# Performance work log

Measured on AMD Instinct MI355X. Metric: run time of the kernel, lower is better.

The kernel has to match this reference:

```python
import jax, jax.numpy as jnp
import numpy as np

N = 50000      # nodes
E = 640000     # edges
D = 64         # embedding_dim
H1, H2 = 64, 128
EA = 8         # edge_attr_dim
OUT = 4
G = 64         # graphs in batch
NEG_SLOPE = 0.2  # PyG GeneralConv leaky_relu slope


def seg_softmax(a, seg, n):
    # softmax of per-edge scores a grouped by destination node seg
    m = jax.ops.segment_max(a, seg, num_segments=n)
    m = jnp.where(jnp.isfinite(m), m, 0.0)
    e = jnp.exp(a - m[seg])
    s = jax.ops.segment_sum(e, seg, num_segments=n)
    return e / (s[seg] + 1e-16)


def general_conv(h, src, dst, edge_attr, Wm, bm, We, be, att, Ws, bs, n):
    # message: lin_msg(x_j) + lin_edge(edge_attr)   [E, out]
    m = h[src] @ Wm + bm + edge_attr @ We + be
    # additive attention (heads=1): alpha = leaky_relu(<m, att>), softmax per dst
    a = jax.nn.leaky_relu(m @ att, NEG_SLOPE)
    a = seg_softmax(a, dst, n)
    msg = m * a[:, None]
    # scatter-mean aggregate
    s = jax.ops.segment_sum(msg, dst, num_segments=n)
    cnt = jax.ops.segment_sum(jnp.ones_like(a), dst, num_segments=n)
    agg = s / jnp.maximum(cnt, 1.0)[:, None]
    # skip linear on self features
    return agg + h @ Ws + bs


def setup_inputs() -> dict:
    key = jax.random.key(0)
    ks = jax.random.split(key, 24)
    rn = lambda k, shp, sc=0.05: (jax.random.normal(k, shp, jnp.float32) * sc)
    inp = {
        "x": jnp.arange(N),
        "edge_index": jax.random.randint(ks[0], (2, E), 0, N),
        "edge_attr": jax.random.normal(ks[1], (E, EA), jnp.float32),
        "batchh": jnp.sort(jax.random.randint(ks[2], (N,), 0, G)),
        "emb": rn(ks[3], (N, D), 0.1),
        # layer 0: D -> H1
        "Wm0": rn(ks[4], (D, H1)), "bm0": rn(ks[5], (H1,)),
        "We0": rn(ks[6], (EA, H1)), "be0": rn(ks[7], (H1,)),
        "att0": rn(ks[8], (H1,)),
        "Ws0": rn(ks[9], (D, H1)), "bs0": rn(ks[10], (H1,)),
        # layer 1: H1 -> H2
        "Wm1": rn(ks[11], (H1, H2)), "bm1": rn(ks[12], (H2,)),
        "We1": rn(ks[13], (EA, H2)), "be1": rn(ks[14], (H2,)),
        "att1": rn(ks[15], (H2,)),
        "Ws1": rn(ks[16], (H1, H2)), "bs1": rn(ks[17], (H2,)),
        # classifier
        "Wc1": rn(ks[18], (H2, H2)), "bc1": rn(ks[19], (H2,)),
        "Wc2": rn(ks[20], (H2, OUT)), "bc2": rn(ks[21], (OUT,)),
    }
    return inp


def reference(x, edge_index, edge_attr, batchh, emb,
              Wm0, bm0, We0, be0, att0, Ws0, bs0,
              Wm1, bm1, We1, be1, att1, Ws1, bs1,
              Wc1, bc1, Wc2, bc2):
    src, dst = edge_index[0], edge_index[1]
    h = emb[x]                                   # [N, D]
    h = jax.nn.relu(general_conv(h, src, dst, edge_attr, Wm0, bm0, We0, be0, att0, Ws0, bs0, N))
    h = jax.nn.relu(general_conv(h, src, dst, edge_attr, Wm1, bm1, We1, be1, att1, Ws1, bs1, N))
    # global mean pool per graph (dropout is identity in eval)
    s = jax.ops.segment_sum(h, batchh, num_segments=G)
    c = jax.ops.segment_sum(jnp.ones((h.shape[0],), h.dtype), batchh, num_segments=G)
    g = s / jnp.maximum(c, 1.0)[:, None]         # [G, H2]
    return jax.nn.relu(g @ Wc1 + bc1) @ Wc2 + bc2  # [G, OUT]
```

## Files before the change

kernel.cpp:

```cpp
#include <hip/hip_runtime.h>
#include <hip/hip_bf16.h>

#define DEV_INLINE __device__ __forceinline__

static constexpr int WAVE = 64;
static constexpr int EB   = 2048;
static constexpr int CAP  = 4096;
static constexpr float FP8_SCALE = 64.0f;
static constexpr float FP8_INV   = 1.0f / 64.0f;
static constexpr float EA_SCALE  = 8.0f;
static constexpr float EA_INV    = 1.0f / 8.0f;

typedef float floatx2 __attribute__((ext_vector_type(2)));
typedef unsigned int uintx4 __attribute__((ext_vector_type(4)));

DEV_INLINE float leaky02(float x) { return x > 0.f ? x : 0.2f * x; }
DEV_INLINE unsigned short f2b(float f) {
    __hip_bfloat16 b = __float2bfloat16(f);
    return *reinterpret_cast<unsigned short*>(&b);
}
DEV_INLINE float b2f(unsigned short u) {
    unsigned int x = ((unsigned int)u) << 16;
    return __uint_as_float(x);
}

__global__ __launch_bounds__(256)
void stage_kernel(const int* __restrict__ ei, const float* __restrict__ ea, int E, int nbuck,
                  const float* __restrict__ We0, const float* __restrict__ att0,
                  const float* __restrict__ be0,
                  const float* __restrict__ We1, const float* __restrict__ att1,
                  const float* __restrict__ be1,
                  int* __restrict__ bucket_cursor, unsigned int* __restrict__ staging) {
    __shared__ float swatt[32];
    __shared__ int hist[256];
    __shared__ int basesh[256];
    int tid = threadIdx.x;

    if (tid < 9) {
        float s = 0.f;
        if (tid < 8) { for (int h = 0; h < 64; ++h) s += We0[tid * 64 + h] * att0[h]; }
        else         { for (int h = 0; h < 64; ++h) s += be0[h] * att0[h]; }
        swatt[tid] = s;
    } else if (tid >= 16 && tid < 25) {
        int k = tid - 16;
        float s = 0.f;
        if (k < 8) { for (int h = 0; h < 128; ++h) s += We1[k * 128 + h] * att1[h]; }
        else       { for (int h = 0; h < 128; ++h) s += be1[h] * att1[h]; }
        swatt[tid] = s;
    }
    hist[tid] = 0;
    __syncthreads();

    int e0 = blockIdx.x * EB;
    constexpr int EPT = EB / 256;
    int rank[EPT];
    #pragma unroll
    for (int j = 0; j < EPT; ++j) {
        int e = e0 + j * 256 + tid;
        rank[j] = 0;
        if (e < E) {
            int b = ei[E + e] >> 8;
            rank[j] = atomicAdd(&hist[b], 1);
        }
    }
    __syncthreads();
    basesh[tid] = (hist[tid] > 0 && tid < nbuck) ? atomicAdd(&bucket_cursor[tid], hist[tid]) : 0;
    __syncthreads();

    #pragma unroll
    for (int j = 0; j < EPT; ++j) {
        int e = e0 + j * 256 + tid;
        if (e >= E) continue;
        int d = ei[E + e];
        int src = ei[e];
        int b = d >> 8;
        const float4* p = reinterpret_cast<const float4*>(ea + (size_t)e * 8);
        float4 a0 = p[0], a1 = p[1];
        float s0 = swatt[8]
                 + a0.x * swatt[0] + a0.y * swatt[1] + a0.z * swatt[2] + a0.w * swatt[3]
                 + a1.x * swatt[4] + a1.y * swatt[5] + a1.z * swatt[6] + a1.w * swatt[7];
        float s1 = swatt[24]
                 + a0.x * swatt[16] + a0.y * swatt[17] + a0.z * swatt[18] + a0.w * swatt[19]
                 + a1.x * swatt[20] + a1.y * swatt[21] + a1.z * swatt[22] + a1.w * swatt[23];
        int lo = 0, hi = 0;
        lo = __builtin_amdgcn_cvt_pk_fp8_f32(a0.x * EA_SCALE, a0.y * EA_SCALE, lo, false);
        lo = __builtin_amdgcn_cvt_pk_fp8_f32(a0.z * EA_SCALE, a0.w * EA_SCALE, lo, true);
        hi = __builtin_amdgcn_cvt_pk_fp8_f32(a1.x * EA_SCALE, a1.y * EA_SCALE, hi, false);
        hi = __builtin_amdgcn_cvt_pk_fp8_f32(a1.z * EA_SCALE, a1.w * EA_SCALE, hi, true);
        int pos = basesh[b] + rank[j];
        if (pos >= CAP) continue;
        uintx4 pk;
        pk[0] = (unsigned int)(src & 0xffff) | ((unsigned int)(d & 255) << 16);
        pk[1] = (unsigned int)f2b(s0) | ((unsigned int)f2b(s1) << 16);
        pk[2] = (unsigned int)lo;
        pk[3] = (unsigned int)hi;
        *reinterpret_cast<uintx4*>(staging + ((size_t)b * CAP + pos) * 4) = pk;
    }
}

__global__ __launch_bounds__(256)
void bucket_scan_kernel(const int* __restrict__ bucket_cursor, int nbuck,
                        int* __restrict__ bucket_base, int* __restrict__ csroff,
                        int N, int E) {
    __shared__ int ws2[4];
    int t = threadIdx.x, lane = t & 63, wid = t >> 6;
    int v = (t < nbuck) ? bucket_cursor[t] : 0;
    int incl = v;
    #pragma unroll
    for (int o = 1; o < 64; o <<= 1) { int u = __shfl_up(incl, o); if (lane >= o) incl += u; }
    if (lane == 63) ws2[wid] = incl;
    __syncthreads();
    int woff = 0;
    for (int w0 = 0; w0 < wid; ++w0) woff += ws2[w0];
    if (t < nbuck) bucket_base[t] = woff + incl - v;
    if (t == 0) csroff[N] = E;
}

__global__ __launch_bounds__(256)
void place_kernel(const unsigned int* __restrict__ staging,
                  const int* __restrict__ bucket_cursor, const int* __restrict__ bucket_base,
                  int* __restrict__ csroff, unsigned int* __restrict__ packed, int N) {
    __shared__ int deg[256];
    __shared__ int wsum[4];
    int b = blockIdx.x;
    int tid = threadIdx.x, lane = tid & 63, wid = tid >> 6;
    deg[tid] = 0;
    __syncthreads();
    int cnt = min(bucket_cursor[b], CAP);
    int base = bucket_base[b];
    const unsigned int* st = staging + (size_t)b * CAP * 4;

    for (int i = tid; i < cnt; i += 256) {
        unsigned int w0 = st[(size_t)i * 4];
        atomicAdd(&deg[(w0 >> 16) & 255], 1);
    }
    __syncthreads();
    int v = deg[tid];
    int incl = v;
    #pragma unroll
    for (int o = 1; o < 64; o <<= 1) { int u = __shfl_up(incl, o); if (lane >= o) incl += u; }
    if (lane == 63) wsum[wid] = incl;
    __syncthreads();
    int woff = 0;
    for (int w0 = 0; w0 < wid; ++w0) woff += wsum[w0];
    int excl = woff + incl - v;
    int node = b * 256 + tid;
    if (node < N) csroff[node] = base + excl;
    __syncthreads();
    deg[tid] = excl;
    __syncthreads();
    for (int i = tid; i < cnt; i += 256) {
        const uintx4 pk = *reinterpret_cast<const uintx4*>(st + (size_t)i * 4);
        int dl = (pk[0] >> 16) & 255;
        int pos = base + atomicAdd(&deg[dl], 1);
        *reinterpret_cast<uintx4*>(packed + (size_t)pos * 4) = pk;
    }
}

template <int H, int NB, bool INBF16>
__global__ __launch_bounds__(256)
void nodelin_kernel(const float* __restrict__ hf, const unsigned short* __restrict__ hb,
                    const int* __restrict__ xidx,
                    const float* __restrict__ Wm, const float* __restrict__ bm,
                    const float* __restrict__ Ws, const float* __restrict__ bs,
                    const float* __restrict__ att,
                    unsigned char* __restrict__ hWm8, unsigned short* __restrict__ hWsb,
                    float* __restrict__ nscore, int n) {
    constexpr int F4  = H / 4;
    constexpr int NC  = 256 / F4;
    constexpr int NPT = NB / NC;
    constexpr int LDW = 68;
    __shared__ float sh[NB][LDW];
    int n0 = blockIdx.x * NB;
    int tid = threadIdx.x;

    for (int i = tid; i < NB * 16; i += 256) {
        int node = i >> 4, q = i & 15;
        int row = n0 + node;
        float4 v = make_float4(0.f, 0.f, 0.f, 0.f);
        if (row < n) {
            if constexpr (INBF16) {
                ushort4 u = reinterpret_cast<const ushort4*>(hb + (size_t)row * 64)[q];
                v = make_float4(b2f(u.x), b2f(u.y), b2f(u.z), b2f(u.w));
            } else {
                int src = xidx ? xidx[row] : row;
                v = reinterpret_cast<const float4*>(hf + (size_t)src * 64)[q];
            }
        }
        reinterpret_cast<float4*>(&sh[node][0])[q] = v;
    }
    __syncthreads();

    int f4 = (tid % F4) * 4;
    int j0 = tid / F4;
    float4 am[NPT], as[NPT];
    float4 bm4 = *reinterpret_cast<const float4*>(bm + f4);
    float4 bs4 = *reinterpret_cast<const float4*>(bs + f4);
    #pragma unroll
    for (int p = 0; p < NPT; ++p) { am[p] = bm4; as[p] = bs4; }

    for (int k4 = 0; k4 < 16; ++k4) {
        float4 hv[NPT];
        #pragma unroll
        for (int p = 0; p < NPT; ++p)
            hv[p] = reinterpret_cast<const float4*>(&sh[j0 + p * NC][0])[k4];
        #pragma unroll
        for (int kk = 0; kk < 4; ++kk) {
            int k = k4 * 4 + kk;
            float4 wm = *reinterpret_cast<const float4*>(Wm + k * H + f4);
            float4 ws = *reinterpret_cast<const float4*>(Ws + k * H + f4);
            #pragma unroll
            for (int p = 0; p < NPT; ++p) {
                float hk = (&hv[p].x)[kk];
                am[p].x += hk * wm.x; am[p].y += hk * wm.y;
                am[p].z += hk * wm.z; am[p].w += hk * wm.w;
                as[p].x += hk * ws.x; as[p].y += hk * ws.y;
                as[p].z += hk * ws.z; as[p].w += hk * ws.w;
            }
        }
    }

    float4 at4 = *reinterpret_cast<const float4*>(att + f4);
    #pragma unroll
    for (int p = 0; p < NPT; ++p) {
        int row = n0 + j0 + p * NC;
        float sc = am[p].x * at4.x + am[p].y * at4.y + am[p].z * at4.z + am[p].w * at4.w;
        #pragma unroll
        for (int o = 1; o < F4; o <<= 1) sc += __shfl_xor(sc, o);
        if (row < n) {
            int pk = 0;
            pk = __builtin_amdgcn_cvt_pk_fp8_f32(am[p].x * FP8_SCALE, am[p].y * FP8_SCALE, pk, false);
            pk = __builtin_amdgcn_cvt_pk_fp8_f32(am[p].z * FP8_SCALE, am[p].w * FP8_SCALE, pk, true);
            *reinterpret_cast<unsigned int*>(hWm8 + (size_t)row * H + f4) = (unsigned int)pk;
            ushort4 sb;
            sb.x = f2b(as[p].x); sb.y = f2b(as[p].y); sb.z = f2b(as[p].z); sb.w = f2b(as[p].w);
            *reinterpret_cast<ushort4*>(hWsb + (size_t)row * H + f4) = sb;
            if ((tid % F4) == 0) nscore[row] = sc;
        }
    }
}

template <int H, int L>
__global__ __launch_bounds__(256)
void agg_kernel(const int* __restrict__ csr_off, const uint4* __restrict__ packed,
                const float* __restrict__ nscore,
                const float* __restrict__ We, const float* __restrict__ be,
                const unsigned char* __restrict__ hWm8, const unsigned short* __restrict__ hWsb,
                unsigned short* __restrict__ hout, int n) {
    constexpr int LSUB = (H == 128) ? 32 : 16;
    constexpr int NPW  = 64 / LSUB;
    constexpr int NPB  = NPW * 4;
    constexpr int MAXC = 64 / LSUB;
    int tid  = threadIdx.x;
    int lane = tid & 63;
    int wv   = tid >> 6;
    int sg   = lane / LSUB;
    int l    = lane % LSUB;
    int node = blockIdx.x * NPB + wv * NPW + sg;
    if (node >= n) return;
    int base = lane - l;
    int off0 = csr_off[node];
    int deg  = csr_off[node + 1] - off0;

    if (deg == 0) {
        ushort4 hs = *reinterpret_cast<const ushort4*>(hWsb + (size_t)node * H + 4 * l);
        ushort4 ob;
        ob.x = f2b(fmaxf(b2f(hs.x), 0.f));
        ob.y = f2b(fmaxf(b2f(hs.y), 0.f));
        ob.z = f2b(fmaxf(b2f(hs.z), 0.f));
        ob.w = f2b(fmaxf(b2f(hs.w), 0.f));
        *reinterpret_cast<ushort4*>(hout + (size_t)node * H + 4 * l) = ob;
        return;
    }

    float acc4[4] = {0.f, 0.f, 0.f, 0.f};
    float cea8[8] = {0.f, 0.f, 0.f, 0.f, 0.f, 0.f, 0.f, 0.f};

    auto gather_batch = [&](int se_c, float cf_c, int cnt) {
        for (int j0 = 0; j0 < cnt; j0 += 8) {
            float cj[8];
            unsigned int gj[8];
            #pragma unroll
            for (int u = 0; u < 8; ++u) {
                int j = j0 + u;
                int jj = (j < cnt) ? j : 0;
                int sj = __shfl(se_c, base + jj);
                float cf_ = __shfl(cf_c, base + jj);
                cj[u] = (j < cnt) ? cf_ : 0.f;
                gj[u] = *reinterpret_cast<const unsigned int*>(
                    hWm8 + (size_t)sj * H + 4 * l);
            }
            #pragma unroll
            for (int u = 0; u < 8; ++u) {
                floatx2 lo = __builtin_amdgcn_cvt_pk_f32_fp8(gj[u], false);
                floatx2 hi = __builtin_amdgcn_cvt_pk_f32_fp8(gj[u], true);
                acc4[0] += cj[u] * lo[0];
                acc4[1] += cj[u] * lo[1];
                acc4[2] += cj[u] * hi[0];
                acc4[3] += cj[u] * hi[1];
            }
        }
    };

    if (deg <= MAXC * LSUB) {
        int se[MAXC];
        float cf[MAXC];
        unsigned int g0[MAXC], g1[MAXC];
        float mx = -1e30f;
        #pragma unroll
        for (int c = 0; c < MAXC; ++c) {
            int i = c * LSUB + l;
            se[c] = 0; g0[c] = 0; g1[c] = 0;
            float sc = -1e30f;
            if (i < deg) {
                uint4 pk = packed[off0 + i];
                se[c] = (int)(pk.x & 0xffffu);
                float eaw = b2f((unsigned short)((pk.y >> (L * 16)) & 0xffff));
                sc = leaky02(nscore[se[c]] + eaw);
                g0[c] = pk.z; g1[c] = pk.w;
            }
            cf[c] = sc;
            mx = fmaxf(mx, sc);
        }
        #pragma unroll
        for (int o = LSUB / 2; o > 0; o >>= 1) mx = fmaxf(mx, __shfl_xor(mx, o));
        float ssum = 0.f;
        #pragma unroll
        for (int c = 0; c < MAXC; ++c) {
            int i = c * LSUB + l;
            float e = (i < deg) ? __expf(cf[c] - mx) : 0.f;
            cf[c] = e;
            ssum += e;
        }
        #pragma unroll
        for (int o = LSUB / 2; o > 0; o >>= 1) ssum += __shfl_xor(ssum, o);
        float invs = 1.f / (ssum + 1e-16f);

        #pragma unroll
        for (int c = 0; c < MAXC; ++c) {
            cf[c] *= invs;
            float cj = cf[c];
            if (cj > 0.f) {
                floatx2 p0 = __builtin_amdgcn_cvt_pk_f32_fp8(g0[c], false);
                floatx2 p1 = __builtin_amdgcn_cvt_pk_f32_fp8(g0[c], true);
                floatx2 p2 = __builtin_amdgcn_cvt_pk_f32_fp8(g1[c], false);
                floatx2 p3 = __builtin_amdgcn_cvt_pk_f32_fp8(g1[c], true);
                cea8[0] += cj * p0[0]; cea8[1] += cj * p0[1];
                cea8[2] += cj * p1[0]; cea8[3] += cj * p1[1];
                cea8[4] += cj * p2[0]; cea8[5] += cj * p2[1];
                cea8[6] += cj * p3[0]; cea8[7] += cj * p3[1];
            }
        }
        #pragma unroll
        for (int c = 0; c < MAXC; ++c) {
            int cnt = min(LSUB, deg - c * LSUB);
            gather_batch(se[c], cf[c], cnt);
            if ((c + 1) * LSUB >= deg) break;
        }
    } else {
        float mx = -1e30f;
        for (int i = l; i < deg; i += LSUB) {
            uint4 pk = packed[off0 + i];
            float eaw = b2f((unsigned short)((pk.y >> (L * 16)) & 0xffff));
            mx = fmaxf(mx, leaky02(nscore[(int)(pk.x & 0xffffu)] + eaw));
        }
        #pragma unroll
        for (int o = LSUB / 2; o > 0; o >>= 1) mx = fmaxf(mx, __shfl_xor(mx, o));
        float ssum = 0.f;
        for (int i = l; i < deg; i += LSUB) {
            uint4 pk = packed[off0 + i];
            float eaw = b2f((unsigned short)((pk.y >> (L * 16)) & 0xffff));
            ssum += __expf(leaky02(nscore[(int)(pk.x & 0xffffu)] + eaw) - mx);
        }
        #pragma unroll
        for (int o = LSUB / 2; o > 0; o >>= 1) ssum += __shfl_xor(ssum, o);
        float invs = 1.f / (ssum + 1e-16f);

        for (int c0 = 0; c0 < deg; c0 += LSUB) {
            int cnt = min(LSUB, deg - c0);
            int se = 0;
            float cf = 0.f;
            if (l < cnt) {
                uint4 pk = packed[off0 + c0 + l];
                se = (int)(pk.x & 0xffffu);
                float eaw = b2f((unsigned short)((pk.y >> (L * 16)) & 0xffff));
                cf = __expf(leaky02(nscore[se] + eaw) - mx) * invs;
                floatx2 p0 = __builtin_amdgcn_cvt_pk_f32_fp8(pk.z, false);
                floatx2 p1 = __builtin_amdgcn_cvt_pk_f32_fp8(pk.z, true);
                floatx2 p2 = __builtin_amdgcn_cvt_pk_f32_fp8(pk.w, false);
                floatx2 p3 = __builtin_amdgcn_cvt_pk_f32_fp8(pk.w, true);
                cea8[0] += cf * p0[0]; cea8[1] += cf * p0[1];
                cea8[2] += cf * p1[0]; cea8[3] += cf * p1[1];
                cea8[4] += cf * p2[0]; cea8[5] += cf * p2[1];
                cea8[6] += cf * p3[0]; cea8[7] += cf * p3[1];
            }
            gather_batch(se, cf, cnt);
        }
    }

    #pragma unroll
    for (int k = 0; k < 8; ++k) {
        float v = cea8[k];
        #pragma unroll
        for (int o = LSUB / 2; o > 0; o >>= 1) v += __shfl_xor(v, o);
        cea8[k] = v * EA_INV;
    }

    float invdeg = 1.f / (float)deg;
    ushort4 hs = *reinterpret_cast<const ushort4*>(hWsb + (size_t)node * H + 4 * l);
    float sk[4] = {b2f(hs.x), b2f(hs.y), b2f(hs.z), b2f(hs.w)};
    ushort4 ob;
    unsigned short* obp = &ob.x;
    #pragma unroll
    for (int k = 0; k < 4; ++k) {
        int f = 4 * l + k;
        float ew = be[f];
        #pragma unroll
        for (int k8 = 0; k8 < 8; ++k8) ew += cea8[k8] * We[k8 * H + f];
        float v = (acc4[k] * FP8_INV + ew) * invdeg + sk[k];
        obp[k] = f2b(fmaxf(v, 0.f));
    }
    *reinterpret_cast<ushort4*>(hout + (size_t)node * H + 4 * l) = ob;
}

__global__ __launch_bounds__(128)
void pool_sum_kernel(const unsigned short* __restrict__ h, const int* __restrict__ batchh,
                     float* __restrict__ gsum, int n) {
    int f = threadIdx.x;
    int chunk = (n + gridDim.x - 1) / gridDim.x;
    int start = blockIdx.x * chunk;
    int end = min(n, start + chunk);
    if (start >= end) return;
    float acc = 0.f;
    int cur = batchh[start];
    for (int node = start; node < end; ++node) {
        int b = batchh[node];
        if (b != cur) {
            atomicAdd(&gsum[cur * 128 + f], acc);
            acc = 0.f;
            cur = b;
        }
        acc += b2f(h[(size_t)node * 128 + f]);
    }
    atomicAdd(&gsum[cur * 128 + f], acc);
}

__global__ __launch_bounds__(128)
void classifier_kernel(const float* __restrict__ gsum, const int* __restrict__ batchh, int n,
                       const float* __restrict__ Wc1, const float* __restrict__ bc1,
                       const float* __restrict__ Wc2, const float* __restrict__ bc2,
                       float* __restrict__ out) {
    int b = blockIdx.x;
    int f = threadIdx.x;
    __shared__ float gm[128];
    __shared__ float t1[128];
    __shared__ int cnt;
    if (f == 0) {
        auto lb = [&](int key) {
            int lo = 0, hi = n;
            while (lo < hi) {
                int mid = (lo + hi) >> 1;
                if (batchh[mid] < key) lo = mid + 1; else hi = mid;
            }
            return lo;
        };
        cnt = lb(b + 1) - lb(b);
    }
    __syncthreads();
    float c = (float)max(cnt, 1);
    gm[f] = gsum[b * 128 + f] / c;
    __syncthreads();
    float acc = bc1[f];
    for (int k = 0; k < 128; ++k) acc += gm[k] * Wc1[k * 128 + f];
    t1[f] = fmaxf(acc, 0.f);
    __syncthreads();
    if (f < 4) {
        float o = bc2[f];
        for (int k = 0; k < 128; ++k) o += t1[k] * Wc2[k * 4 + f];
        out[b * 4 + f] = o;
    }
}

extern "C" void kernel_launch(void* const* d_in, const int* in_sizes, int n_in,
                              void* d_out, int out_size, void* d_ws, size_t ws_size,
                              hipStream_t stream) {
    const int* x      = (const int*)d_in[0];
    const int* ei     = (const int*)d_in[1];
    const float* ea   = (const float*)d_in[2];
    const int* batchh = (const int*)d_in[3];
    const float* emb  = (const float*)d_in[4];
    const float* Wm0 = (const float*)d_in[5];  const float* bm0 = (const float*)d_in[6];
    const float* We0 = (const float*)d_in[7];  const float* be0 = (const float*)d_in[8];
    const float* att0 = (const float*)d_in[9];
    const float* Ws0 = (const float*)d_in[10]; const float* bs0 = (const float*)d_in[11];
    const float* Wm1 = (const float*)d_in[12]; const float* bm1 = (const float*)d_in[13];
    const float* We1 = (const float*)d_in[14]; const float* be1 = (const float*)d_in[15];
    const float* att1 = (const float*)d_in[16];
    const float* Ws1 = (const float*)d_in[17]; const float* bs1 = (const float*)d_in[18];
    const float* Wc1 = (const float*)d_in[19]; const float* bc1 = (const float*)d_in[20];
    const float* Wc2 = (const float*)d_in[21]; const float* bc2 = (const float*)d_in[22];

    const int N = in_sizes[0];
    const int E = in_sizes[1] / 2;
    const int G = 64;
    const int H2 = 128;
    const int NBUCK = (N + 255) >> 8;

    char* w = (char*)d_ws;
    auto alloc = [&](size_t bytes) -> void* {
        void* p = (void*)w;
        w += (bytes + 255) & ~(size_t)255;
        return p;
    };
    unsigned short* hbuf  = (unsigned short*)alloc((size_t)N * 128 * 2);
    unsigned char* hWm8   = (unsigned char*)alloc((size_t)N * 128);
    unsigned short* hWsb  = (unsigned short*)alloc((size_t)N * 128 * 2);
    float* nscore         = (float*)alloc((size_t)N * 4);
    unsigned int* packed  = (unsigned int*)alloc((size_t)E * 16);
    unsigned int* staging = (unsigned int*)alloc((size_t)NBUCK * CAP * 16);
    int* bucket_cursor    = (int*)alloc(256 * 4);
    int* bucket_base      = (int*)alloc(256 * 4);
    int* csroff           = (int*)alloc((size_t)(N + 1) * 4);
    float* gsum           = (float*)alloc((size_t)G * H2 * 4);

    auto cdiv = [](int a, int b) { return (a + b - 1) / b; };

    (void)hipMemsetAsync(bucket_cursor, 0, 256 * 4, stream);
    (void)hipMemsetAsync(gsum, 0, (size_t)G * H2 * 4, stream);

    stage_kernel<<<cdiv(E, EB), 256, 0, stream>>>(ei, ea, E, NBUCK,
                                                  We0, att0, be0, We1, att1, be1,
                                                  bucket_cursor, staging);
    bucket_scan_kernel<<<1, 256, 0, stream>>>(bucket_cursor, NBUCK, bucket_base, csroff, N, E);
    place_kernel<<<NBUCK, 256, 0, stream>>>(staging, bucket_cursor, bucket_base,
                                            csroff, packed, N);

    nodelin_kernel<64, 64, false><<<cdiv(N, 64), 256, 0, stream>>>(
        emb, nullptr, x, Wm0, bm0, Ws0, bs0, att0, hWm8, hWsb, nscore, N);
    agg_kernel<64, 0><<<cdiv(N, 16), 256, 0, stream>>>(csroff, (const uint4*)packed, nscore,
                                                       We0, be0, hWm8, hWsb, hbuf, N);

    nodelin_kernel<128, 32, true><<<cdiv(N, 32), 256, 0, stream>>>(
        nullptr, hbuf, nullptr, Wm1, bm1, Ws1, bs1, att1, hWm8, hWsb, nscore, N);
    agg_kernel<128, 1><<<cdiv(N, 8), 256, 0, stream>>>(csroff, (const uint4*)packed, nscore,
                                                       We1, be1, hWm8, hWsb, hbuf, N);

    pool_sum_kernel<<<512, 128, 0, stream>>>(hbuf, batchh, gsum, N);
    classifier_kernel<<<G, 128, 0, stream>>>(gsum, batchh, N, Wc1, bc1, Wc2, bc2, (float*)d_out);
}
```

Before: 310.8 us.

## Fuse staging with layer-0 node linear, fold scan into place, fuse pooling into agg

Merges the edge staging kernel and the layer-0 node linear into one launch by splitting the grid between them. Each place block now computes its own bucket base with a reduction, which removes the separate scan kernel. The layer-1 aggregation now accumulates the global mean pool directly into 8 replicated per-graph sums through shared memory and atomics, so the final node features are never written and the pool kernel is gone. Launch count and global traffic drop, at the cost of extra atomics and shared-memory work in the aggregation kernel.

New measurement: 268.6 us. -13.6%, faster.

```diff
diff --git a/kernel.cpp b/kernel.cpp
--- a/kernel.cpp
+++ b/kernel.cpp
@@ -6,6 +6,7 @@
 static constexpr int WAVE = 64;
 static constexpr int EB   = 2048;
 static constexpr int CAP  = 4096;
+static constexpr int GREP = 8;
 static constexpr float FP8_SCALE = 64.0f;
 static constexpr float FP8_INV   = 1.0f / 64.0f;
 static constexpr float EA_SCALE  = 8.0f;
@@ -24,16 +25,17 @@
     return __uint_as_float(x);
 }
 
-__global__ __launch_bounds__(256)
-void stage_kernel(const int* __restrict__ ei, const float* __restrict__ ea, int E, int nbuck,
-                  const float* __restrict__ We0, const float* __restrict__ att0,
-                  const float* __restrict__ be0,
-                  const float* __restrict__ We1, const float* __restrict__ att1,
-                  const float* __restrict__ be1,
-                  int* __restrict__ bucket_cursor, unsigned int* __restrict__ staging) {
-    __shared__ float swatt[32];
-    __shared__ int hist[256];
-    __shared__ int basesh[256];
+DEV_INLINE void stage_body(char* smemraw, int bx,
+                           const int* __restrict__ ei, const float* __restrict__ ea,
+                           int E, int nbuck,
+                           const float* __restrict__ We0, const float* __restrict__ att0,
+                           const float* __restrict__ be0,
+                           const float* __restrict__ We1, const float* __restrict__ att1,
+                           const float* __restrict__ be1,
+                           int* __restrict__ bucket_cursor, unsigned int* __restrict__ staging) {
+    float* swatt = reinterpret_cast<float*>(smemraw);
+    int* hist    = reinterpret_cast<int*>(smemraw + 128);
+    int* basesh  = reinterpret_cast<int*>(smemraw + 128 + 1024);
     int tid = threadIdx.x;
 
     if (tid < 9) {
@@ -51,7 +53,7 @@
     hist[tid] = 0;
     __syncthreads();
 
-    int e0 = blockIdx.x * EB;
+    int e0 = bx * EB;
     constexpr int EPT = EB / 256;
     int rank[EPT];
     #pragma unroll
@@ -98,80 +100,21 @@
     }
 }
 
-__global__ __launch_bounds__(256)
-void bucket_scan_kernel(const int* __restrict__ bucket_cursor, int nbuck,
-                        int* __restrict__ bucket_base, int* __restrict__ csroff,
-                        int N, int E) {
-    __shared__ int ws2[4];
-    int t = threadIdx.x, lane = t & 63, wid = t >> 6;
-    int v = (t < nbuck) ? bucket_cursor[t] : 0;
-    int incl = v;
-    #pragma unroll
-    for (int o = 1; o < 64; o <<= 1) { int u = __shfl_up(incl, o); if (lane >= o) incl += u; }
-    if (lane == 63) ws2[wid] = incl;
-    __syncthreads();
-    int woff = 0;
-    for (int w0 = 0; w0 < wid; ++w0) woff += ws2[w0];
-    if (t < nbuck) bucket_base[t] = woff + incl - v;
-    if (t == 0) csroff[N] = E;
-}
-
-__global__ __launch_bounds__(256)
-void place_kernel(const unsigned int* __restrict__ staging,
-                  const int* __restrict__ bucket_cursor, const int* __restrict__ bucket_base,
-                  int* __restrict__ csroff, unsigned int* __restrict__ packed, int N) {
-    __shared__ int deg[256];
-    __shared__ int wsum[4];
-    int b = blockIdx.x;
-    int tid = threadIdx.x, lane = tid & 63, wid = tid >> 6;
-    deg[tid] = 0;
-    __syncthreads();
-    int cnt = min(bucket_cursor[b], CAP);
-    int base = bucket_base[b];
-    const unsigned int* st = staging + (size_t)b * CAP * 4;
-
-    for (int i = tid; i < cnt; i += 256) {
-        unsigned int w0 = st[(size_t)i * 4];
-        atomicAdd(&deg[(w0 >> 16) & 255], 1);
-    }
-    __syncthreads();
-    int v = deg[tid];
-    int incl = v;
-    #pragma unroll
-    for (int o = 1; o < 64; o <<= 1) { int u = __shfl_up(incl, o); if (lane >= o) incl += u; }
-    if (lane == 63) wsum[wid] = incl;
-    __syncthreads();
-    int woff = 0;
-    for (int w0 = 0; w0 < wid; ++w0) woff += wsum[w0];
-    int excl = woff + incl - v;
-    int node = b * 256 + tid;
-    if (node < N) csroff[node] = base + excl;
-    __syncthreads();
-    deg[tid] = excl;
-    __syncthreads();
-    for (int i = tid; i < cnt; i += 256) {
-        const uintx4 pk = *reinterpret_cast<const uintx4*>(st + (size_t)i * 4);
-        int dl = (pk[0] >> 16) & 255;
-        int pos = base + atomicAdd(&deg[dl], 1);
-        *reinterpret_cast<uintx4*>(packed + (size_t)pos * 4) = pk;
-    }
-}
-
 template <int H, int NB, bool INBF16>
-__global__ __launch_bounds__(256)
-void nodelin_kernel(const float* __restrict__ hf, const unsigned short* __restrict__ hb,
-                    const int* __restrict__ xidx,
-                    const float* __restrict__ Wm, const float* __restrict__ bm,
-                    const float* __restrict__ Ws, const float* __restrict__ bs,
-                    const float* __restrict__ att,
-                    unsigned char* __restrict__ hWm8, unsigned short* __restrict__ hWsb,
-                    float* __restrict__ nscore, int n) {
+DEV_INLINE void nodelin_body(char* smemraw, int bx,
+                             const float* __restrict__ hf, const unsigned short* __restrict__ hb,
+                             const int* __restrict__ xidx,
+                             const float* __restrict__ Wm, const float* __restrict__ bm,
+                             const float* __restrict__ Ws, const float* __restrict__ bs,
+                             const float* __restrict__ att,
+                             unsigned char* __restrict__ hWm8, unsigned short* __restrict__ hWsb,
+                             float* __restrict__ nscore, int n) {
     constexpr int F4  = H / 4;
     constexpr int NC  = 256 / F4;
     constexpr int NPT = NB / NC;
     constexpr int LDW = 68;
-    __shared__ float sh[NB][LDW];
-    int n0 = blockIdx.x * NB;
+    float (*sh)[LDW] = reinterpret_cast<float (*)[LDW]>(smemraw);
+    int n0 = bx * NB;
     int tid = threadIdx.x;
 
     for (int i = tid; i < NB * 16; i += 256) {
@@ -240,213 +183,316 @@
     }
 }
 
-template <int H, int L>
+__global__ __launch_bounds__(256)
+void stage_nodelin0_kernel(const int* __restrict__ ei, const float* __restrict__ ea,
+                           int E, int nbuck, int stage_blocks,
+                           const float* __restrict__ We0, const float* __restrict__ att0,
+                           const float* __restrict__ be0,
+                           const float* __restrict__ We1, const float* __restrict__ att1,
+                           const float* __restrict__ be1,
+                           int* __restrict__ bucket_cursor, unsigned int* __restrict__ staging,
+                           const float* __restrict__ emb, const int* __restrict__ xidx,
+                           const float* __restrict__ Wm0, const float* __restrict__ bm0,
+                           const float* __restrict__ Ws0, const float* __restrict__ bs0,
+                           unsigned char* __restrict__ hWm8, unsigned short* __restrict__ hWsb,
+                           float* __restrict__ nscore, int n) {
+    __shared__ alignas(16) char smem[64 * 68 * 4];
+    if ((int)blockIdx.x < stage_blocks) {
+        stage_body(smem, blockIdx.x, ei, ea, E, nbuck, We0, att0, be0, We1, att1, be1,
+                   bucket_cursor, staging);
+    } else {
+        nodelin_body<64, 64, false>(smem, blockIdx.x - stage_blocks, emb, nullptr, xidx,
+                                    Wm0, bm0, Ws0, bs0, att0, hWm8, hWsb, nscore, n);
+    }
+}
+
+template <int H, int NB, bool INBF16>
+__global__ __launch_bounds__(256)
+void nodelin_kernel(const float* __restrict__ hf, const unsigned short* __restrict__ hb,
+                    const int* __restrict__ xidx,
+                    const float* __restrict__ Wm, const float* __restrict__ bm,
+                    const float* __restrict__ Ws, const float* __restrict__ bs,
+                    const float* __restrict__ att,
+                    unsigned char* __restrict__ hWm8, unsigned short* __restrict__ hWsb,
+                    float* __restrict__ nscore, int n) {
+    __shared__ alignas(16) char smem[NB * 68 * 4];
+    nodelin_body<H, NB, INBF16>(smem, blockIdx.x, hf, hb, xidx, Wm, bm, Ws, bs, att,
+                                hWm8, hWsb, nscore, n);
+}
+
+__global__ __launch_bounds__(256)
+void place_kernel(const unsigned int* __restrict__ staging,
+                  const int* __restrict__ bucket_cursor,
+                  int* __restrict__ csroff, unsigned int* __restrict__ packed,
+                  int N, int E, int nbuck) {
+    __shared__ int deg[256];
+    __shared__ int wsum[4];
+    __shared__ int bsum[4];
+    int b = blockIdx.x;
+    int tid = threadIdx.x, lane = tid & 63, wid = tid >> 6;
+
+    int vb = (tid < b) ? bucket_cursor[tid] : 0;
+    #pragma unroll
+    for (int o = 1; o < 64; o <<= 1) vb += __shfl_xor(vb, o);
+    if (lane == 0) bsum[wid] = vb;
+    deg[tid] = 0;
+    __syncthreads();
+    int base = bsum[0] + bsum[1] + bsum[2] + bsum[3];
+
+    int cnt = min(bucket_cursor[b], CAP);
+    const unsigned int* st = staging + (size_t)b * CAP * 4;
+
+    for (int i = tid; i < cnt; i += 256) {
+        unsigned int w0 = st[(size_t)i * 4];
+        atomicAdd(&deg[(w0 >> 16) & 255], 1);
+    }
+    __syncthreads();
+    int v = deg[tid];
+    int incl = v;
+    #pragma unroll
+    for (int o = 1; o < 64; o <<= 1) { int u = __shfl_up(incl, o); if (lane >= o) incl += u; }
+    if (lane == 63) wsum[wid] = incl;
+    __syncthreads();
+    int woff = 0;
+    for (int w0 = 0; w0 < wid; ++w0) woff += wsum[w0];
+    int excl = woff + incl - v;
+    int node = b * 256 + tid;
+    if (node < N) csroff[node] = base + excl;
+    if (b == 0 && tid == 0) csroff[N] = E;
+    __syncthreads();
+    deg[tid] = excl;
+    __syncthreads();
+    for (int i = tid; i < cnt; i += 256) {
+        const uintx4 pk = *reinterpret_cast<const uintx4*>(st + (size_t)i * 4);
+        int dl = (pk[0] >> 16) & 255;
+        int pos = base + atomicAdd(&deg[dl], 1);
+        *reinterpret_cast<uintx4*>(packed + (size_t)pos * 4) = pk;
+    }
+}
+
+template <int H, int L, bool POOL>
 __global__ __launch_bounds__(256)
 void agg_kernel(const int* __restrict__ csr_off, const uint4* __restrict__ packed,
                 const float* __restrict__ nscore,
                 const float* __restrict__ We, const float* __restrict__ be,
                 const unsigned char* __restrict__ hWm8, const unsigned short* __restrict__ hWsb,
-                unsigned short* __restrict__ hout, int n) {
+                unsigned short* __restrict__ hout,
+                const int* __restrict__ batchh, float* __restrict__ gsumR, int n) {
     constexpr int LSUB = (H == 128) ? 32 : 16;
     constexpr int NPW  = 64 / LSUB;
     constexpr int NPB  = NPW * 4;
     constexpr int MAXC = 64 / LSUB;
+    constexpr int GR   = POOL ? NPB : 1;
+    __shared__ float gacc[GR][128];
+    __shared__ int gofs[GR];
     int tid  = threadIdx.x;
     int lane = tid & 63;
     int wv   = tid >> 6;
     int sg   = lane / LSUB;
     int l    = lane % LSUB;
-    int node = blockIdx.x * NPB + wv * NPW + sg;
-    if (node >= n) return;
-    int base = lane - l;
-    int off0 = csr_off[node];
-    int deg  = csr_off[node + 1] - off0;
-
-    if (deg == 0) {
-        ushort4 hs = *reinterpret_cast<const ushort4*>(hWsb + (size_t)node * H + 4 * l);
-        ushort4 ob;
-        ob.x = f2b(fmaxf(b2f(hs.x), 0.f));
-        ob.y = f2b(fmaxf(b2f(hs.y), 0.f));
-        ob.z = f2b(fmaxf(b2f(hs.z), 0.f));
-        ob.w = f2b(fmaxf(b2f(hs.w), 0.f));
-        *reinterpret_cast<ushort4*>(hout + (size_t)node * H + 4 * l) = ob;
-        return;
-    }
-
-    float acc4[4] = {0.f, 0.f, 0.f, 0.f};
-    float cea8[8] = {0.f, 0.f, 0.f, 0.f, 0.f, 0.f, 0.f, 0.f};
-
-    auto gather_batch = [&](int se_c, float cf_c, int cnt) {
-        for (int j0 = 0; j0 < cnt; j0 += 8) {
-            float cj[8];
-            unsigned int gj[8];
+    int sid  = wv * NPW + sg;
+    int node = blockIdx.x * NPB + sid;
+    bool active = node < n;
+    if constexpr (!POOL) { if (!active) return; }
+
+    float vout[4] = {0.f, 0.f, 0.f, 0.f};
+    int g = -1;
+
+    if (active) {
+        int base = lane - l;
+        int off0 = csr_off[node];
+        int deg  = csr_off[node + 1] - off0;
+
+        if (deg == 0) {
+            ushort4 hs = *reinterpret_cast<const ushort4*>(hWsb + (size_t)node * H + 4 * l);
+            vout[0] = fmaxf(b2f(hs.x), 0.f);
+            vout[1] = fmaxf(b2f(hs.y), 0.f);
+            vout[2] = fmaxf(b2f(hs.z), 0.f);
+            vout[3] = fmaxf(b2f(hs.w), 0.f);
+        } else {
+            float acc4[4] = {0.f, 0.f, 0.f, 0.f};
+            float cea8[8] = {0.f, 0.f, 0.f, 0.f, 0.f, 0.f, 0.f, 0.f};
+
+            auto gather_batch = [&](int se_c, float cf_c, int cnt) {
+                for (int j0 = 0; j0 < cnt; j0 += 8) {
+                    float cj[8];
+                    unsigned int gj[8];
+                    #pragma unroll
+                    for (int u = 0; u < 8; ++u) {
+                        int j = j0 + u;
+                        int jj = (j < cnt) ? j : 0;
+                        int sj = __shfl(se_c, base + jj);
+                        float cf_ = __shfl(cf_c, base + jj);
+                        cj[u] = (j < cnt) ? cf_ : 0.f;
+                        gj[u] = *reinterpret_cast<const unsigned int*>(
+                            hWm8 + (size_t)sj * H + 4 * l);
+                    }
+                    #pragma unroll
+                    for (int u = 0; u < 8; ++u) {
+                        floatx2 lo = __builtin_amdgcn_cvt_pk_f32_fp8(gj[u], false);
+                        floatx2 hi = __builtin_amdgcn_cvt_pk_f32_fp8(gj[u], true);
+                        acc4[0] += cj[u] * lo[0];
+                        acc4[1] += cj[u] * lo[1];
+                        acc4[2] += cj[u] * hi[0];
+                        acc4[3] += cj[u] * hi[1];
+                    }
+                }
+            };
+
+            if (deg <= MAXC * LSUB) {
+                int se[MAXC];
+                float cf[MAXC];
+                unsigned int g0[MAXC], g1[MAXC];
+                float mx = -1e30f;
+                #pragma unroll
+                for (int c = 0; c < MAXC; ++c) {
+                    int i = c * LSUB + l;
+                    se[c] = 0; g0[c] = 0; g1[c] = 0;
+                    float sc = -1e30f;
+                    if (i < deg) {
+                        uint4 pk = packed[off0 + i];
+                        se[c] = (int)(pk.x & 0xffffu);
+                        float eaw = b2f((unsigned short)((pk.y >> (L * 16)) & 0xffff));
+                        sc = leaky02(nscore[se[c]] + eaw);
+                        g0[c] = pk.z; g1[c] = pk.w;
+                    }
+                    cf[c] = sc;
+                    mx = fmaxf(mx, sc);
+                }
+                #pragma unroll
+                for (int o = LSUB / 2; o > 0; o >>= 1) mx = fmaxf(mx, __shfl_xor(mx, o));
+                float ssum = 0.f;
+                #pragma unroll
+                for (int c = 0; c < MAXC; ++c) {
+                    int i = c * LSUB + l;
+                    float e = (i < deg) ? __expf(cf[c] - mx) : 0.f;
+                    cf[c] = e;
+                    ssum += e;
+                }
+                #pragma unroll
+                for (int o = LSUB / 2; o > 0; o >>= 1) ssum += __shfl_xor(ssum, o);
+                float invs = 1.f / (ssum + 1e-16f);
+
+                #pragma unroll
+                for (int c = 0; c < MAXC; ++c) {
+                    cf[c] *= invs;
+                    float cj = cf[c];
+                    if (cj > 0.f) {
+                        floatx2 p0 = __builtin_amdgcn_cvt_pk_f32_fp8(g0[c], false);
+                        floatx2 p1 = __builtin_amdgcn_cvt_pk_f32_fp8(g0[c], true);
+                        floatx2 p2 = __builtin_amdgcn_cvt_pk_f32_fp8(g1[c], false);
+                        floatx2 p3 = __builtin_amdgcn_cvt_pk_f32_fp8(g1[c], true);
+                        cea8[0] += cj * p0[0]; cea8[1] += cj * p0[1];
+                        cea8[2] += cj * p1[0]; cea8[3] += cj * p1[1];
+                        cea8[4] += cj * p2[0]; cea8[5] += cj * p2[1];
+                        cea8[6] += cj * p3[0]; cea8[7] += cj * p3[1];
+                    }
+                }
+                #pragma unroll
+                for (int c = 0; c < MAXC; ++c) {
+                    int cnt = min(LSUB, deg - c * LSUB);
+                    gather_batch(se[c], cf[c], cnt);
+                    if ((c + 1) * LSUB >= deg) break;
+                }
+            } else {
+                float mx = -1e30f;
+                for (int i = l; i < deg; i += LSUB) {
+                    uint4 pk = packed[off0 + i];
+                    float eaw = b2f((unsigned short)((pk.y >> (L * 16)) & 0xffff));
+                    mx = fmaxf(mx, leaky02(nscore[(int)(pk.x & 0xffffu)] + eaw));
+                }
+                #pragma unroll
+                for (int o = LSUB / 2; o > 0; o >>= 1) mx = fmaxf(mx, __shfl_xor(mx, o));
+                float ssum = 0.f;
+                for (int i = l; i < deg; i += LSUB) {
+                    uint4 pk = packed[off0 + i];
+                    float eaw = b2f((unsigned short)((pk.y >> (L * 16)) & 0xffff));
+                    ssum += __expf(leaky02(nscore[(int)(pk.x & 0xffffu)] + eaw) - mx);
+                }
+                #pragma unroll
+                for (int o = LSUB / 2; o > 0; o >>= 1) ssum += __shfl_xor(ssum, o);
+                float invs = 1.f / (ssum + 1e-16f);
+
+                for (int c0 = 0; c0 < deg; c0 += LSUB) {
+                    int cnt = min(LSUB, deg - c0);
+                    int se = 0;
+                    float cf = 0.f;
+                    if (l < cnt) {
+                        uint4 pk = packed[off0 + c0 + l];
+                        se = (int)(pk.x & 0xffffu);
+                        float eaw = b2f((unsigned short)((pk.y >> (L * 16)) & 0xffff));
+                        cf = __expf(leaky02(nscore[se] + eaw) - mx) * invs;
+                        floatx2 p0 = __builtin_amdgcn_cvt_pk_f32_fp8(pk.z, false);
+                        floatx2 p1 = __builtin_amdgcn_cvt_pk_f32_fp8(pk.z, true);
+                        floatx2 p2 = __builtin_amdgcn_cvt_pk_f32_fp8(pk.w, false);
+                        floatx2 p3 = __builtin_amdgcn_cvt_pk_f32_fp8(pk.w, true);
+                        cea8[0] += cf * p0[0]; cea8[1] += cf * p0[1];
+                        cea8[2] += cf * p1[0]; cea8[3] += cf * p1[1];
+                        cea8[4] += cf * p2[0]; cea8[5] += cf * p2[1];
+                        cea8[6] += cf * p3[0]; cea8[7] += cf * p3[1];
+                    }
+                    gather_batch(se, cf, cnt);
+                }
+            }
+
             #pragma unroll
-            for (int u = 0; u < 8; ++u) {
-                int j = j0 + u;
-                int jj = (j < cnt) ? j : 0;
-                int sj = __shfl(se_c, base + jj);
-                float cf_ = __shfl(cf_c, base + jj);
-                cj[u] = (j < cnt) ? cf_ : 0.f;
-                gj[u] = *reinterpret_cast<const unsigned int*>(
-                    hWm8 + (size_t)sj * H + 4 * l);
-            }
+            for (int k = 0; k < 8; ++k) {
+                float v = cea8[k];
+                #pragma unroll
+                for (int o = LSUB / 2; o > 0; o >>= 1) v += __shfl_xor(v, o);
+                cea8[k] = v * EA_INV;
+            }
+
+            float invdeg = 1.f / (float)deg;
+            ushort4 hs = *reinterpret_cast<const ushort4*>(hWsb + (size_t)node * H + 4 * l);
+            float sk[4] = {b2f(hs.x), b2f(hs.y), b2f(hs.z), b2f(hs.w)};
             #pragma unroll
-            for (int u = 0; u < 8; ++u) {
-                floatx2 lo = __builtin_amdgcn_cvt_pk_f32_fp8(gj[u], false);
-                floatx2 hi = __builtin_amdgcn_cvt_pk_f32_fp8(gj[u], true);
-                acc4[0] += cj[u] * lo[0];
-                acc4[1] += cj[u] * lo[1];
-                acc4[2] += cj[u] * hi[0];
-                acc4[3] += cj[u] * hi[1];
-            }
-        }
-    };
-
-    if (deg <= MAXC * LSUB) {
-        int se[MAXC];
-        float cf[MAXC];
-        unsigned int g0[MAXC], g1[MAXC];
-        float mx = -1e30f;
+            for (int k = 0; k < 4; ++k) {
+                int f = 4 * l + k;
+                float ew = be[f];
+                #pragma unroll
+                for (int k8 = 0; k8 < 8; ++k8) ew += cea8[k8] * We[k8 * H + f];
+                float v = (acc4[k] * FP8_INV + ew) * invdeg + sk[k];
+                vout[k] = fmaxf(v, 0.f);
+            }
+        }
+
+        if constexpr (!POOL) {
+            ushort4 ob;
+            ob.x = f2b(vout[0]); ob.y = f2b(vout[1]);
+            ob.z = f2b(vout[2]); ob.w = f2b(vout[3]);
+            *reinterpret_cast<ushort4*>(hout + (size_t)node * H + 4 * l) = ob;
+        }
+    }
+
+    if constexpr (POOL) {
+        if (active) g = batchh[node];
         #pragma unroll
-        for (int c = 0; c < MAXC; ++c) {
-            int i = c * LSUB + l;
-            se[c] = 0; g0[c] = 0; g1[c] = 0;
-            float sc = -1e30f;
-            if (i < deg) {
-                uint4 pk = packed[off0 + i];
-                se[c] = (int)(pk.x & 0xffffu);
-                float eaw = b2f((unsigned short)((pk.y >> (L * 16)) & 0xffff));
-                sc = leaky02(nscore[se[c]] + eaw);
-                g0[c] = pk.z; g1[c] = pk.w;
-            }
-            cf[c] = sc;
-            mx = fmaxf(mx, sc);
-        }
+        for (int k = 0; k < 4; ++k) gacc[sid][4 * l + k] = active ? vout[k] : 0.f;
+        if (l == 0) gofs[sid] = g;
+        __syncthreads();
+        int f  = tid & 127;
+        int h0 = (tid >> 7) * (NPB / 2);
+        int rep = blockIdx.x & (GREP - 1);
+        float acc = 0.f;
+        int cur = -1;
         #pragma unroll
-        for (int o = LSUB / 2; o > 0; o >>= 1) mx = fmaxf(mx, __shfl_xor(mx, o));
-        float ssum = 0.f;
-        #pragma unroll
-        for (int c = 0; c < MAXC; ++c) {
-            int i = c * LSUB + l;
-            float e = (i < deg) ? __expf(cf[c] - mx) : 0.f;
-            cf[c] = e;
-            ssum += e;
-        }
-        #pragma unroll
-        for (int o = LSUB / 2; o > 0; o >>= 1) ssum += __shfl_xor(ssum, o);
-        float invs = 1.f / (ssum + 1e-16f);
-
-        #pragma unroll
-        for (int c = 0; c < MAXC; ++c) {
-            cf[c] *= invs;
-            float cj = cf[c];
-            if (cj > 0.f) {
-                floatx2 p0 = __builtin_amdgcn_cvt_pk_f32_fp8(g0[c], false);
-                floatx2 p1 = __builtin_amdgcn_cvt_pk_f32_fp8(g0[c], true);
-                floatx2 p2 = __builtin_amdgcn_cvt_pk_f32_fp8(g1[c], false);
-                floatx2 p3 = __builtin_amdgcn_cvt_pk_f32_fp8(g1[c], true);
-                cea8[0] += cj * p0[0]; cea8[1] += cj * p0[1];
-                cea8[2] += cj * p1[0]; cea8[3] += cj * p1[1];
-                cea8[4] += cj * p2[0]; cea8[5] += cj * p2[1];
-                cea8[6] += cj * p3[0]; cea8[7] += cj * p3[1];
-            }
-        }
-        #pragma unroll
-        for (int c = 0; c < MAXC; ++c) {
-            int cnt = min(LSUB, deg - c * LSUB);
-            gather_batch(se[c], cf[c], cnt);
-            if ((c + 1) * LSUB >= deg) break;
-        }
-    } else {
-        float mx = -1e30f;
-        for (int i = l; i < deg; i += LSUB) {
-            uint4 pk = packed[off0 + i];
-            float eaw = b2f((unsigned short)((pk.y >> (L * 16)) & 0xffff));
-            mx = fmaxf(mx, leaky02(nscore[(int)(pk.x & 0xffffu)] + eaw));
-        }
-        #pragma unroll
-        for (int o = LSUB / 2; o > 0; o >>= 1) mx = fmaxf(mx, __shfl_xor(mx, o));
-        float ssum = 0.f;
-        for (int i = l; i < deg; i += LSUB) {
-            uint4 pk = packed[off0 + i];
-            float eaw = b2f((unsigned short)((pk.y >> (L * 16)) & 0xffff));
-            ssum += __expf(leaky02(nscore[(int)(pk.x & 0xffffu)] + eaw) - mx);
-        }
-        #pragma unroll
-        for (int o = LSUB / 2; o > 0; o >>= 1) ssum += __shfl_xor(ssum, o);
-        float invs = 1.f / (ssum + 1e-16f);
-
-        for (int c0 = 0; c0 < deg; c0 += LSUB) {
-            int cnt = min(LSUB, deg - c0);
-            int se = 0;
-            float cf = 0.f;
-            if (l < cnt) {
-                uint4 pk = packed[off0 + c0 + l];
-                se = (int)(pk.x & 0xffffu);
-                float eaw = b2f((unsigned short)((pk.y >> (L * 16)) & 0xffff));
-                cf = __expf(leaky02(nscore[se] + eaw) - mx) * invs;
-                floatx2 p0 = __builtin_amdgcn_cvt_pk_f32_fp8(pk.z, false);
-                floatx2 p1 = __builtin_amdgcn_cvt_pk_f32_fp8(pk.z, true);
-                floatx2 p2 = __builtin_amdgcn_cvt_pk_f32_fp8(pk.w, false);
-                floatx2 p3 = __builtin_amdgcn_cvt_pk_f32_fp8(pk.w, true);
-                cea8[0] += cf * p0[0]; cea8[1] += cf * p0[1];
-                cea8[2] += cf * p1[0]; cea8[3] += cf * p1[1];
-                cea8[4] += cf * p2[0]; cea8[5] += cf * p2[1];
-                cea8[6] += cf * p3[0]; cea8[7] += cf * p3[1];
-            }
-            gather_batch(se, cf, cnt);
-        }
-    }
-
-    #pragma unroll
-    for (int k = 0; k < 8; ++k) {
-        float v = cea8[k];
-        #pragma unroll
-        for (int o = LSUB / 2; o > 0; o >>= 1) v += __shfl_xor(v, o);
-        cea8[k] = v * EA_INV;
-    }
-
-    float invdeg = 1.f / (float)deg;
-    ushort4 hs = *reinterpret_cast<const ushort4*>(hWsb + (size_t)node * H + 4 * l);
-    float sk[4] = {b2f(hs.x), b2f(hs.y), b2f(hs.z), b2f(hs.w)};
-    ushort4 ob;
-    unsigned short* obp = &ob.x;
-    #pragma unroll
-    for (int k = 0; k < 4; ++k) {
-        int f = 4 * l + k;
-        float ew = be[f];
-        #pragma unroll
-        for (int k8 = 0; k8 < 8; ++k8) ew += cea8[k8] * We[k8 * H + f];
-        float v = (acc4[k] * FP8_INV + ew) * invdeg + sk[k];
-        obp[k] = f2b(fmaxf(v, 0.f));
-    }
-    *reinterpret_cast<ushort4*>(hout + (size_t)node * H + 4 * l) = ob;
+        for (int s = h0; s < h0 + NPB / 2; ++s) {
+            int gg = gofs[s];
+            if (gg < 0) continue;
+            if (gg != cur) {
+                if (cur >= 0) atomicAdd(&gsumR[((size_t)rep * 64 + cur) * 128 + f], acc);
+                cur = gg;
+                acc = 0.f;
+            }
+            acc += gacc[s][f];
+        }
+        if (cur >= 0) atomicAdd(&gsumR[((size_t)rep * 64 + cur) * 128 + f], acc);
+    }
 }
 
 __global__ __launch_bounds__(128)
-void pool_sum_kernel(const unsigned short* __restrict__ h, const int* __restrict__ batchh,
-                     float* __restrict__ gsum, int n) {
-    int f = threadIdx.x;
-    int chunk = (n + gridDim.x - 1) / gridDim.x;
-    int start = blockIdx.x * chunk;
-    int end = min(n, start + chunk);
-    if (start >= end) return;
-    float acc = 0.f;
-    int cur = batchh[start];
-    for (int node = start; node < end; ++node) {
-        int b = batchh[node];
-        if (b != cur) {
-            atomicAdd(&gsum[cur * 128 + f], acc);
-            acc = 0.f;
-            cur = b;
-        }
-        acc += b2f(h[(size_t)node * 128 + f]);
-    }
-    atomicAdd(&gsum[cur * 128 + f], acc);
-}
-
-__global__ __launch_bounds__(128)
-void classifier_kernel(const float* __restrict__ gsum, const int* __restrict__ batchh, int n,
+void classifier_kernel(const float* __restrict__ gsumR, const int* __restrict__ batchh, int n,
                        const float* __restrict__ Wc1, const float* __restrict__ bc1,
                        const float* __restrict__ Wc2, const float* __restrict__ bc2,
                        float* __restrict__ out) {
@@ -468,7 +514,10 @@
     }
     __syncthreads();
     float c = (float)max(cnt, 1);
-    gm[f] = gsum[b * 128 + f] / c;
+    float s = 0.f;
+    #pragma unroll
+    for (int r = 0; r < GREP; ++r) s += gsumR[((size_t)r * 64 + b) * 128 + f];
+    gm[f] = s / c;
     __syncthreads();
     float acc = bc1[f];
     for (int k = 0; k < 128; ++k) acc += gm[k] * Wc1[k * 128 + f];
@@ -503,7 +552,6 @@
     const int N = in_sizes[0];
     const int E = in_sizes[1] / 2;
     const int G = 64;
-    const int H2 = 128;
     const int NBUCK = (N + 255) >> 8;
 
     char* w = (char*)d_ws;
@@ -519,32 +567,30 @@
     unsigned int* packed  = (unsigned int*)alloc((size_t)E * 16);
     unsigned int* staging = (unsigned int*)alloc((size_t)NBUCK * CAP * 16);
     int* bucket_cursor    = (int*)alloc(256 * 4);
-    int* bucket_base      = (int*)alloc(256 * 4);
+    float* gsumR          = (float*)alloc((size_t)GREP * G * 128 * 4);
     int* csroff           = (int*)alloc((size_t)(N + 1) * 4);
-    float* gsum           = (float*)alloc((size_t)G * H2 * 4);
 
     auto cdiv = [](int a, int b) { return (a + b - 1) / b; };
 
-    (void)hipMemsetAsync(bucket_cursor, 0, 256 * 4, stream);
-    (void)hipMemsetAsync(gsum, 0, (size_t)G * H2 * 4, stream);
-
-    stage_kernel<<<cdiv(E, EB), 256, 0, stream>>>(ei, ea, E, NBUCK,
-                                                  We0, att0, be0, We1, att1, be1,
-                                                  bucket_cursor, staging);
-    bucket_scan_kernel<<<1, 256, 0, stream>>>(bucket_cursor, NBUCK, bucket_base, csroff, N, E);
-    place_kernel<<<NBUCK, 256, 0, stream>>>(staging, bucket_cursor, bucket_base,
-                                            csroff, packed, N);
-
-    nodelin_kernel<64, 64, false><<<cdiv(N, 64), 256, 0, stream>>>(
-        emb, nullptr, x, Wm0, bm0, Ws0, bs0, att0, hWm8, hWsb, nscore, N);
-    agg_kernel<64, 0><<<cdiv(N, 16), 256, 0, stream>>>(csroff, (const uint4*)packed, nscore,
-                                                       We0, be0, hWm8, hWsb, hbuf, N);
+    (void)hipMemsetAsync(bucket_cursor, 0, 256 * 4 + (size_t)GREP * G * 128 * 4, stream);
+
+    const int stageB = cdiv(E, EB);
+    const int nl0B   = cdiv(N, 64);
+
+    stage_nodelin0_kernel<<<stageB + nl0B, 256, 0, stream>>>(
+        ei, ea, E, NBUCK, stageB, We0, att0, be0, We1, att1, be1,
+        bucket_cursor, staging, emb, x, Wm0, bm0, Ws0, bs0, hWm8, hWsb, nscore, N);
+
+    place_kernel<<<NBUCK, 256, 0, stream>>>(staging, bucket_cursor, csroff, packed, N, E, NBUCK);
+
+    agg_kernel<64, 0, false><<<cdiv(N, 16), 256, 0, stream>>>(
+        csroff, (const uint4*)packed, nscore, We0, be0, hWm8, hWsb, hbuf, nullptr, nullptr, N);
 
     nodelin_kernel<128, 32, true><<<cdiv(N, 32), 256, 0, stream>>>(
         nullptr, hbuf, nullptr, Wm1, bm1, Ws1, bs1, att1, hWm8, hWsb, nscore, N);
-    agg_kernel<128, 1><<<cdiv(N, 8), 256, 0, stream>>>(csroff, (const uint4*)packed, nscore,
-                                                       We1, be1, hWm8, hWsb, hbuf, N);
-
-    pool_sum_kernel<<<512, 128, 0, stream>>>(hbuf, batchh, gsum, N);
-    classifier_kernel<<<G, 128, 0, stream>>>(gsum, batchh, N, Wc1, bc1, Wc2, bc2, (float*)d_out);
-}
+
+    agg_kernel<128, 1, true><<<cdiv(N, 8), 256, 0, stream>>>(
+        csroff, (const uint4*)packed, nscore, We1, be1, hWm8, hWsb, nullptr, batchh, gsumR, N);
+
+    classifier_kernel<<<G, 128, 0, stream>>>(gsumR, batchh, N, Wc1, bc1, Wc2, bc2, (float*)d_out);
+}
```
